# Optimization experiments

Measured on AMD Instinct MI355X. Metric: run time of the kernel, lower is better.

The kernel has to match this reference:

```python
import jax, jax.numpy as jnp
import numpy as np

B, T, D, H = 4, 1024, 1024, 16
DH = D // H
EPS = 1e-5


def setup_inputs() -> dict:
    key = jax.random.key(0)
    ks = jax.random.split(key, 14)
    sc = 1.0 / np.sqrt(D)
    x = jax.random.normal(ks[0], (B, T, D), jnp.float32)
    W_r = jax.random.normal(ks[1], (D, D), jnp.float32) * sc
    W_k = jax.random.normal(ks[2], (D, D), jnp.float32) * sc
    W_v = jax.random.normal(ks[3], (D, D), jnp.float32) * sc
    W_w = jax.random.normal(ks[4], (D, D), jnp.float32) * sc
    W_o = jax.random.normal(ks[5], (D, D), jnp.float32) * sc
    u = jax.random.normal(ks[6], (H, DH), jnp.float32) * 0.1
    tm_r = jax.random.uniform(ks[7], (D,), jnp.float32)
    tm_k = jax.random.uniform(ks[8], (D,), jnp.float32)
    tm_v = jax.random.uniform(ks[9], (D,), jnp.float32)
    tm_w = jax.random.uniform(ks[10], (D,), jnp.float32)
    ln_w = jnp.ones((DH,), jnp.float32) + 0.1 * jax.random.normal(ks[11], (DH,), jnp.float32)
    ln_b = 0.1 * jax.random.normal(ks[12], (DH,), jnp.float32)
    return {"x": x, "W_r": W_r, "W_k": W_k, "W_v": W_v, "W_w": W_w, "W_o": W_o,
            "u": u, "tm_r": tm_r, "tm_k": tm_k, "tm_v": tm_v, "tm_w": tm_w,
            "ln_w": ln_w, "ln_b": ln_b}


def _rwkv6(x, W_r, W_k, W_v, W_w, W_o, u, tm_r, tm_k, tm_v, tm_w, ln_w, ln_b):
    b, t, d = x.shape
    # token-shift mix
    x_prev = jnp.concatenate([jnp.zeros_like(x[:, :1]), x[:, :-1]], axis=1)
    xr = tm_r * x + (1.0 - tm_r) * x_prev
    xk = tm_k * x + (1.0 - tm_k) * x_prev
    xv = tm_v * x + (1.0 - tm_v) * x_prev
    xw = tm_w * x + (1.0 - tm_w) * x_prev
    r = jax.nn.sigmoid(xr @ W_r.T)          # (B,T,D)
    k = xk @ W_k.T
    v = xv @ W_v.T
    w = -jax.nn.softplus(-(xw @ W_w.T)) - 1e-4  # always < 0 -> exp(w) in (0,1)
    r = r.reshape(b, t, H, DH)
    k = k.reshape(b, t, H, DH)
    v = v.reshape(b, t, H, DH)
    w = w.reshape(b, t, H, DH)

    def step(s, rkvw):
        r_t, k_t, v_t, w_t = rkvw  # each (B,H,DH)
        bonus = jnp.exp(u + k_t)[..., :, None] * v_t[..., None, :]  # (B,H,DH,DH)
        o_t = jnp.einsum('bhi,bhij->bhj', r_t, s + bonus)
        s = jnp.exp(w_t)[..., None] * s + k_t[..., :, None] * v_t[..., None, :]
        return s, o_t

    s0 = jnp.zeros((b, H, DH, DH), x.dtype)
    rkvw = tuple(a.transpose(1, 0, 2, 3) for a in (r, k, v, w))  # (T,B,H,DH)
    _, o = jax.lax.scan(step, s0, rkvw)      # o: (T,B,H,DH)
    o = o.transpose(1, 0, 2, 3)              # (B,T,H,DH)
    # group LayerNorm over head dim
    mu = jnp.mean(o, axis=-1, keepdims=True)
    var = jnp.var(o, axis=-1, keepdims=True)
    o = (o - mu) * jax.lax.rsqrt(var + EPS) * ln_w + ln_b
    o = o * r
    return (o.reshape(b, t, d)) @ W_o.T


def reference(x, W_r, W_k, W_v, W_w, W_o, u, tm_r, tm_k, tm_v, tm_w, ln_w, ln_b):
    return _rwkv6(x, W_r, W_k, W_v, W_w, W_o, u, tm_r, tm_k, tm_v, tm_w, ln_w, ln_b)
```

## Files before the change

kernel.cpp:

```cpp
#include <hip/hip_runtime.h>


typedef unsigned short u16;
typedef unsigned int   u32;

typedef __attribute__((ext_vector_type(8))) __bf16 bf16x8;
typedef __attribute__((ext_vector_type(4))) float   f32x4;

#define MB (1u << 20)

#define LDS_PTR(p) ((__attribute__((address_space(3))) void*)(p))
#define GLB_PTR(p) ((const __attribute__((address_space(1))) void*)(p))

__device__ __forceinline__ u16 f2bf(float f) {
  u32 u = __builtin_bit_cast(u32, f);
  u += 0x7FFFu + ((u >> 16) & 1u);
  return (u16)(u >> 16);
}
__device__ __forceinline__ float bf2f(u16 x) {
  u32 u = ((u32)x) << 16;
  return __builtin_bit_cast(float, u);
}
__device__ __forceinline__ u32 pack2(float a, float b) {
  return (u32)f2bf(a) | ((u32)f2bf(b) << 16);
}

__global__ __launch_bounds__(256) void prep_w(
    const float* __restrict__ w0, const float* __restrict__ w1,
    const float* __restrict__ w2, const float* __restrict__ w3,
    const float* __restrict__ w4, u32* __restrict__ out) {
  int idx = blockIdx.x * 256 + threadIdx.x;
  int m = idx >> 19;
  int l = idx & 524287;
  const float* src = (m == 0) ? w0 : (m == 1) ? w1 : (m == 2) ? w2 : (m == 3) ? w3 : w4;
  float2 v = *(const float2*)(src + (size_t)l * 2);
  out[idx] = pack2(v.x, v.y);
}

__global__ __launch_bounds__(256) void prep_mix(
    const float* __restrict__ x,
    const float* __restrict__ tmr, const float* __restrict__ tmk,
    const float* __restrict__ tmv, const float* __restrict__ tmw,
    u32* __restrict__ xr, u32* __restrict__ xk,
    u32* __restrict__ xv, u32* __restrict__ xw) {
  int idx = blockIdx.x * 256 + threadIdx.x;
  int t  = (idx >> 9) & 1023;
  int d0 = (idx & 511) * 2;
  size_t e = (size_t)idx * 2;
  float2 xc = *(const float2*)(x + e);
  float2 xp = make_float2(0.f, 0.f);
  if (t > 0) xp = *(const float2*)(x + e - 1024);
  float2 tm;
  tm = *(const float2*)(tmr + d0);
  xr[idx] = pack2(tm.x * xc.x + (1.f - tm.x) * xp.x, tm.y * xc.y + (1.f - tm.y) * xp.y);
  tm = *(const float2*)(tmk + d0);
  xk[idx] = pack2(tm.x * xc.x + (1.f - tm.x) * xp.x, tm.y * xc.y + (1.f - tm.y) * xp.y);
  tm = *(const float2*)(tmv + d0);
  xv[idx] = pack2(tm.x * xc.x + (1.f - tm.x) * xp.x, tm.y * xc.y + (1.f - tm.y) * xp.y);
  tm = *(const float2*)(tmw + d0);
  xw[idx] = pack2(tm.x * xc.x + (1.f - tm.x) * xp.x, tm.y * xc.y + (1.f - tm.y) * xp.y);
}

__global__ __launch_bounds__(512, 1) void gemm_proj(
    const u16* __restrict__ xr, const u16* __restrict__ xk,
    const u16* __restrict__ xv, const u16* __restrict__ xw,
    const u16* __restrict__ Wr, const u16* __restrict__ Wk,
    const u16* __restrict__ Wv, const u16* __restrict__ Ww,
    u16* __restrict__ rO, u16* __restrict__ kO,
    u16* __restrict__ vO, float* __restrict__ wO) {
  constexpr int KITER = 16;
  constexpr int LDK   = 1024;
  __shared__ __align__(16) u16 Asm[2 * 16384];
  __shared__ __align__(16) u16 Bsm[2 * 16384];

  int mat = blockIdx.z;
  const u16* A = (mat == 0) ? xr : (mat == 1) ? xk : (mat == 2) ? xv : xw;
  const u16* W = (mat == 0) ? Wr : (mat == 1) ? Wk : (mat == 2) ? Wv : Ww;

  int tid = threadIdx.x;
  int m0 = blockIdx.x * 256, n0 = blockIdx.y * 256;
  int wave = tid >> 6, lane = tid & 63;
  int wm = (wave >> 2) * 128;
  int wn = (wave & 3) * 64;
  int r16 = lane & 15, quad = lane >> 4;

  f32x4 acc[8][4] = {};

  int lrow  = lane >> 3;
  int lchk  = (lane & 7) ^ lrow;
  const u16* Ag[4];
  const u16* Bg[4];
#pragma unroll
  for (int i = 0; i < 4; ++i) {
    int row = wave * 32 + i * 8 + lrow;
    Ag[i] = A + (size_t)(m0 + row) * LDK + lchk * 8;
    Bg[i] = W + (size_t)(n0 + row) * LDK + lchk * 8;
  }
  int ldsW = wave * 2048;

  int aoff[8], boff[4];
#pragma unroll
  for (int mt = 0; mt < 8; ++mt) {
    int r = wm + mt * 16 + r16;
    aoff[mt] = r * 64 + (quad ^ (r16 & 7)) * 8;
  }
#pragma unroll
  for (int nt = 0; nt < 4; ++nt) {
    int r = wn + nt * 16 + r16;
    boff[nt] = r * 64 + (quad ^ (r16 & 7)) * 8;
  }

#define ISSUE_TILE(t, buf)                                                              \
  do {                                                                                  \
    int _o = (buf) * 16384 + ldsW, _k = (t) * 64;                                       \
    __builtin_amdgcn_global_load_lds(GLB_PTR(Ag[0] + _k), LDS_PTR(Asm + _o),        16, 0, 0); \
    __builtin_amdgcn_global_load_lds(GLB_PTR(Ag[1] + _k), LDS_PTR(Asm + _o + 512),  16, 0, 0); \
    __builtin_amdgcn_global_load_lds(GLB_PTR(Ag[2] + _k), LDS_PTR(Asm + _o + 1024), 16, 0, 0); \
    __builtin_amdgcn_global_load_lds(GLB_PTR(Ag[3] + _k), LDS_PTR(Asm + _o + 1536), 16, 0, 0); \
    __builtin_amdgcn_global_load_lds(GLB_PTR(Bg[0] + _k), LDS_PTR(Bsm + _o),        16, 0, 0); \
    __builtin_amdgcn_global_load_lds(GLB_PTR(Bg[1] + _k), LDS_PTR(Bsm + _o + 512),  16, 0, 0); \
    __builtin_amdgcn_global_load_lds(GLB_PTR(Bg[2] + _k), LDS_PTR(Bsm + _o + 1024), 16, 0, 0); \
    __builtin_amdgcn_global_load_lds(GLB_PTR(Bg[3] + _k), LDS_PTR(Bsm + _o + 1536), 16, 0, 0); \
  } while (0)

  ISSUE_TILE(0, 0);
  ISSUE_TILE(1, 1);

  int cur = 0;
  for (int i = 0; i < KITER; ++i) {
    if (i < KITER - 1) asm volatile("s_waitcnt vmcnt(8)" ::: "memory");
    else               asm volatile("s_waitcnt vmcnt(0)" ::: "memory");
    __builtin_amdgcn_s_barrier();

    const u16* As = Asm + cur * 16384;
    const u16* Bs = Bsm + cur * 16384;
#pragma unroll
    for (int kk = 0; kk < 2; ++kk) {
      int kx = kk * 32;
      bf16x8 af[8], bfm[4];
#pragma unroll
      for (int mt = 0; mt < 8; ++mt) af[mt] = *(const bf16x8*)&As[aoff[mt] ^ kx];
#pragma unroll
      for (int nt = 0; nt < 4; ++nt) bfm[nt] = *(const bf16x8*)&Bs[boff[nt] ^ kx];
#pragma unroll
      for (int mt = 0; mt < 8; ++mt)
#pragma unroll
        for (int nt = 0; nt < 4; ++nt)
          acc[mt][nt] = __builtin_amdgcn_mfma_f32_16x16x32_bf16(af[mt], bfm[nt], acc[mt][nt], 0, 0, 0);
    }

    asm volatile("s_waitcnt lgkmcnt(0)" ::: "memory");
    __builtin_amdgcn_s_barrier();
    if (i + 2 < KITER) ISSUE_TILE(i + 2, cur);
    cur ^= 1;
  }
#undef ISSUE_TILE

#pragma unroll
  for (int mt = 0; mt < 8; ++mt) {
#pragma unroll
    for (int nt = 0; nt < 4; ++nt) {
#pragma unroll
      for (int rg = 0; rg < 4; ++rg) {
        int row = m0 + wm + mt * 16 + quad * 4 + rg;
        int col = n0 + wn + nt * 16 + r16;
        float v = acc[mt][nt][rg];
        size_t idx = (size_t)row * 1024 + col;
        if (mat == 0)      rO[idx] = f2bf(1.f / (1.f + __expf(-v)));
        else if (mat == 1) kO[idx] = f2bf(v);
        else if (mat == 2) vO[idx] = f2bf(v);
        else               wO[idx] = v;
      }
    }
  }
}

template <int KITER>
__device__ __forceinline__ void gemm_core(
    const u16* __restrict__ A, const u16* __restrict__ W, float* __restrict__ O,
    u16* Asm, u16* Bsm) {
  constexpr int LDK = KITER * 32;
  int tid = threadIdx.x;
  int m0 = blockIdx.x * 128, n0 = blockIdx.y * 128;
  int wave = tid >> 6, lane = tid & 63;
  int wm = (wave >> 1) * 64, wn = (wave & 1) * 64;
  int r16 = lane & 15, quad = lane >> 4;

  f32x4 acc[4][4] = {};

  int srow0 = wave * 32 + (lane >> 2);
  int srow1 = srow0 + 16;
  int c4    = lane & 3;
  int q0 = c4 ^ ((srow0 >> 1) & 3);
  int q1 = c4 ^ ((srow1 >> 1) & 3);
  const u16* Ag0 = A + (size_t)(m0 + srow0) * LDK + q0 * 8;
  const u16* Ag1 = A + (size_t)(m0 + srow1) * LDK + q1 * 8;
  const u16* Bg0 = W + (size_t)(n0 + srow0) * LDK + q0 * 8;
  const u16* Bg1 = W + (size_t)(n0 + srow1) * LDK + q1 * 8;
  int ldsOff0 = wave * 1024;
  int ldsOff1 = wave * 1024 + 512;

  int aoff[4], boff[4];
#pragma unroll
  for (int mt = 0; mt < 4; ++mt) {
    int r = wm + mt * 16 + r16;
    aoff[mt] = r * 32 + (quad ^ ((r >> 1) & 3)) * 8;
  }
#pragma unroll
  for (int nt = 0; nt < 4; ++nt) {
    int r = wn + nt * 16 + r16;
    boff[nt] = r * 32 + (quad ^ ((r >> 1) & 3)) * 8;
  }

#define ISSUE_TILE(t, buf)                                                              \
  do {                                                                                  \
    int _o = (buf) * 4096, _k = (t) * 32;                                               \
    __builtin_amdgcn_global_load_lds(GLB_PTR(Ag0 + _k), LDS_PTR(Asm + _o + ldsOff0), 16, 0, 0); \
    __builtin_amdgcn_global_load_lds(GLB_PTR(Ag1 + _k), LDS_PTR(Asm + _o + ldsOff1), 16, 0, 0); \
    __builtin_amdgcn_global_load_lds(GLB_PTR(Bg0 + _k), LDS_PTR(Bsm + _o + ldsOff0), 16, 0, 0); \
    __builtin_amdgcn_global_load_lds(GLB_PTR(Bg1 + _k), LDS_PTR(Bsm + _o + ldsOff1), 16, 0, 0); \
  } while (0)

  ISSUE_TILE(0, 0);
  ISSUE_TILE(1, 1);
  ISSUE_TILE(2, 2);

  int cur = 0;
  for (int i = 0; i < KITER; ++i) {
    if (i < KITER - 2)       asm volatile("s_waitcnt vmcnt(8)" ::: "memory");
    else if (i == KITER - 2) asm volatile("s_waitcnt vmcnt(4)" ::: "memory");
    else                     asm volatile("s_waitcnt vmcnt(0)" ::: "memory");
    __builtin_amdgcn_s_barrier();

    const u16* As = Asm + cur * 4096;
    const u16* Bs = Bsm + cur * 4096;
    bf16x8 af[4], bfm[4];
#pragma unroll
    for (int mt = 0; mt < 4; ++mt) af[mt] = *(const bf16x8*)&As[aoff[mt]];
#pragma unroll
    for (int nt = 0; nt < 4; ++nt) bfm[nt] = *(const bf16x8*)&Bs[boff[nt]];
#pragma unroll
    for (int mt = 0; mt < 4; ++mt)
#pragma unroll
      for (int nt = 0; nt < 4; ++nt)
        acc[mt][nt] = __builtin_amdgcn_mfma_f32_16x16x32_bf16(af[mt], bfm[nt], acc[mt][nt], 0, 0, 0);

    asm volatile("s_waitcnt lgkmcnt(0)" ::: "memory");
    __builtin_amdgcn_s_barrier();
    if (i + 3 < KITER) ISSUE_TILE(i + 3, cur);
    cur = (cur == 2) ? 0 : cur + 1;
  }
#undef ISSUE_TILE

#pragma unroll
  for (int mt = 0; mt < 4; ++mt)
#pragma unroll
    for (int nt = 0; nt < 4; ++nt)
#pragma unroll
      for (int rg = 0; rg < 4; ++rg) {
        int row = m0 + wm + mt * 16 + quad * 4 + rg;
        int col = n0 + wn + nt * 16 + r16;
        O[(size_t)row * 1024 + col] = acc[mt][nt][rg];
      }
}

__global__ __launch_bounds__(256) void gemm_out(
    const u16* __restrict__ A, const u16* __restrict__ W, float* __restrict__ O) {
  __shared__ __align__(16) u16 Asm[3 * 4096];
  __shared__ __align__(16) u16 Bsm[3 * 4096];
  gemm_core<32>(A, W, O, Asm, Bsm);
}

__global__ __launch_bounds__(256) void scan_intra(
    const u16* __restrict__ rb, const u16* __restrict__ kb,
    const u16* __restrict__ vb, const float* __restrict__ wb,
    const float* __restrict__ u,
    float* __restrict__ o, u16* __restrict__ rd,
    float* __restrict__ U, float* __restrict__ Dc) {
  int c = blockIdx.x, bh = blockIdx.y;
  int b = bh >> 4, h = bh & 15;
  int tid = threadIdx.x, ig = tid >> 6, j = tid & 63;

  __shared__ __align__(16) float4 combo[4][64];
  __shared__ float vs_[4][64];
  __shared__ float part[4][4][64];

  const float EW_SCALE = 0.99990001f;

  float s[16];
#pragma unroll
  for (int ii = 0; ii < 16; ++ii) s[ii] = 0.f;

  size_t base = ((size_t)(b * 1024 + c * 32)) * 1024 + h * 64 + j;
  float dloc = 1.0f;
  float uval = (ig < 2) ? u[h * 64 + j] : 0.f;

#define STAGE(t2, sl)                                                     \
  do {                                                                    \
    size_t _idx = base + (size_t)(t2) * 1024;                             \
    if (ig < 2) {                                                         \
      float _r = bf2f(rb[_idx]);                                          \
      float _k = bf2f(kb[_idx]);                                          \
      float _z = wb[_idx];                                                \
      combo[sl][j] = make_float4(_r, _k, __expf(uval + _k),               \
                                 EW_SCALE / (1.f + __expf(-_z)));         \
    } else {                                                              \
      vs_[sl][j] = bf2f(vb[_idx]);                                        \
    }                                                                     \
  } while (0)

  { int p = ig & 1; STAGE(p, p); }
  __syncthreads();

  for (int tt = 0; tt < 32; tt += 2) {
    if (tt + 2 < 32) {
      int p = ig & 1;
      int t2 = tt + 2 + p;
      STAGE(t2, t2 & 3);
    }
#pragma unroll
    for (int p = 0; p < 2; ++p) {
      int t = tt + p, sl = t & 3;
      float vj = vs_[sl][j];
      float acc = 0.f;
#pragma unroll
      for (int ii = 0; ii < 16; ++ii) {
        float4 cb = combo[sl][ig * 16 + ii];
        float tmp = fmaf(cb.z, vj, s[ii]);
        acc = fmaf(cb.x, tmp, acc);
        s[ii] = fmaf(cb.w, s[ii], cb.y * vj);
      }
      part[sl][ig][j] = acc;
      if (ig == 0) {
        float4 me = combo[sl][j];
        rd[base + (size_t)t * 1024] = f2bf(me.x * dloc);
        dloc *= me.w;
      }
    }
    if (tt >= 2) {
      if (ig == 2) {
        int t = tt - 2, sl = t & 3;
        o[base + (size_t)t * 1024] =
            part[sl][0][j] + part[sl][1][j] + part[sl][2][j] + part[sl][3][j];
      } else if (ig == 3) {
        int t = tt - 1, sl = t & 3;
        o[base + (size_t)t * 1024] =
            part[sl][0][j] + part[sl][1][j] + part[sl][2][j] + part[sl][3][j];
      }
    }
    __syncthreads();
  }
#undef STAGE
  if (ig == 2) {
    o[base + (size_t)30 * 1024] = part[2][0][j] + part[2][1][j] + part[2][2][j] + part[2][3][j];
  } else if (ig == 3) {
    o[base + (size_t)31 * 1024] = part[3][0][j] + part[3][1][j] + part[3][2][j] + part[3][3][j];
  }

  float* Ug = U + (size_t)(bh * 32 + c) * 4096;
#pragma unroll
  for (int ii = 0; ii < 16; ++ii) Ug[(ig * 16 + ii) * 64 + j] = s[ii];
  if (ig == 0) Dc[(bh * 32 + c) * 64 + j] = dloc;
}

__global__ __launch_bounds__(256) void state_prop(
    float* __restrict__ U, const float* __restrict__ Dc) {
  int bh  = blockIdx.x >> 4;
  int e   = (blockIdx.x & 15) * 256 + threadIdx.x;
  int i   = e >> 6;
  float acc = 0.f;
  for (int c = 0; c < 32; ++c) {
    float* Ug = U + (size_t)(bh * 32 + c) * 4096 + e;
    float d = Dc[(bh * 32 + c) * 64 + i];
    float uv = *Ug;
    *Ug = acc;
    acc = fmaf(d, acc, uv);
  }
}

__global__ __launch_bounds__(128) void inter_ln(
    const float* __restrict__ o, const u16* __restrict__ rd,
    const u16* __restrict__ rb, const float* __restrict__ U,
    const float* __restrict__ lnw, const float* __restrict__ lnb,
    u16* __restrict__ oh) {
  int c = blockIdx.x, bh = blockIdx.y;
  int b = bh >> 4, h = bh & 15;
  int tid = threadIdx.x, wave = tid >> 6, lane = tid & 63;
  int l15 = lane & 15, quad = lane >> 4;

  __shared__ __align__(16) u16 Sb[64][72];

  const float* Sg = U + (size_t)(bh * 32 + c) * 4096;
#pragma unroll
  for (int q = 0; q < 32; ++q) {
    int e = q * 128 + tid;
    Sb[e & 63][e >> 6] = f2bf(Sg[e]);
  }
  __syncthreads();

  size_t rbase = ((size_t)(b * 1024 + c * 32)) * 1024 + h * 64;

  const u16* rdg = rd + rbase + (size_t)(wave * 16 + l15) * 1024 + quad * 8;
  bf16x8 af0 = *(const bf16x8*)(rdg);
  bf16x8 af1 = *(const bf16x8*)(rdg + 32);

  f32x4 acc[4] = {};
#pragma unroll
  for (int nt = 0; nt < 4; ++nt) {
    const u16* bp = &Sb[nt * 16 + l15][quad * 8];
    bf16x8 b0 = *(const bf16x8*)bp;
    bf16x8 b1 = *(const bf16x8*)(bp + 32);
    acc[nt] = __builtin_amdgcn_mfma_f32_16x16x32_bf16(af0, b0, acc[nt], 0, 0, 0);
    acc[nt] = __builtin_amdgcn_mfma_f32_16x16x32_bf16(af1, b1, acc[nt], 0, 0, 0);
  }

#pragma unroll
  for (int rg = 0; rg < 4; ++rg) {
    int t = wave * 16 + quad * 4 + rg;
    size_t rowb = rbase + (size_t)t * 1024;
    float v[4];
    float s1 = 0.f, s2 = 0.f;
#pragma unroll
    for (int nt = 0; nt < 4; ++nt) {
      v[nt] = acc[nt][rg] + o[rowb + nt * 16 + l15];
      s1 += v[nt];
      s2 += v[nt] * v[nt];
    }
#pragma unroll
    for (int m = 1; m < 16; m <<= 1) {
      s1 += __shfl_xor(s1, m, 64);
      s2 += __shfl_xor(s2, m, 64);
    }
    float mu  = s1 * (1.f / 64.f);
    float var = s2 * (1.f / 64.f) - mu * mu;
    float rstd = rsqrtf(var + 1e-5f);
#pragma unroll
    for (int nt = 0; nt < 4; ++nt) {
      int jj = nt * 16 + l15;
      float nv = (v[nt] - mu) * rstd;
      float val = (nv * lnw[jj] + lnb[jj]) * bf2f(rb[rowb + jj]);
      oh[rowb + jj] = f2bf(val);
    }
  }
}

extern "C" void kernel_launch(void* const* d_in, const int* in_sizes, int n_in,
                              void* d_out, int out_size, void* d_ws, size_t ws_size,
                              hipStream_t stream) {
  const float* x    = (const float*)d_in[0];
  const float* W_r  = (const float*)d_in[1];
  const float* W_k  = (const float*)d_in[2];
  const float* W_v  = (const float*)d_in[3];
  const float* W_w  = (const float*)d_in[4];
  const float* W_o  = (const float*)d_in[5];
  const float* u    = (const float*)d_in[6];
  const float* tm_r = (const float*)d_in[7];
  const float* tm_k = (const float*)d_in[8];
  const float* tm_v = (const float*)d_in[9];
  const float* tm_w = (const float*)d_in[10];
  const float* ln_w = (const float*)d_in[11];
  const float* ln_b = (const float*)d_in[12];
  float* out = (float*)d_out;

  char* ws = (char*)d_ws;
  u16* xr = (u16*)(ws + (size_t)0 * MB);
  u16* xk = (u16*)(ws + (size_t)8 * MB);
  u16* xv = (u16*)(ws + (size_t)16 * MB);
  u16* xw = (u16*)(ws + (size_t)24 * MB);
  float* Ubuf = (float*)(ws + (size_t)0 * MB);
  u16* Wb = (u16*)(ws + (size_t)32 * MB);
  u16* Wrb = Wb;
  u16* Wkb = (u16*)(ws + (size_t)34 * MB);
  u16* Wvb = (u16*)(ws + (size_t)36 * MB);
  u16* Wwb = (u16*)(ws + (size_t)38 * MB);
  u16* Wob = (u16*)(ws + (size_t)40 * MB);
  float* Dcbuf = (float*)(ws + (size_t)42 * MB);
  u16*   rbuf = (u16*)(ws + (size_t)48 * MB);
  u16*   kbuf = (u16*)(ws + (size_t)56 * MB);
  u16*   vbuf = (u16*)(ws + (size_t)64 * MB);
  float* wbuf = (float*)(ws + (size_t)72 * MB);
  float* obuf = (float*)(ws + (size_t)88 * MB);
  u16*  rdbuf = (u16*)(ws + (size_t)104 * MB);
  u16*   ohbuf = (u16*)(ws + (size_t)129 * MB);

  prep_w<<<10240, 256, 0, stream>>>(W_r, W_k, W_v, W_w, W_o, (u32*)Wb);
  prep_mix<<<8192, 256, 0, stream>>>(x, tm_r, tm_k, tm_v, tm_w,
                                     (u32*)xr, (u32*)xk, (u32*)xv, (u32*)xw);
  gemm_proj<<<dim3(16, 4, 4), 512, 0, stream>>>(xr, xk, xv, xw,
                                                Wrb, Wkb, Wvb, Wwb,
                                                rbuf, kbuf, vbuf, wbuf);
  scan_intra<<<dim3(32, 64), 256, 0, stream>>>(rbuf, kbuf, vbuf, wbuf, u,
                                               obuf, rdbuf, Ubuf, Dcbuf);
  state_prop<<<1024, 256, 0, stream>>>(Ubuf, Dcbuf);
  inter_ln<<<dim3(32, 64), 128, 0, stream>>>(obuf, rdbuf, rbuf, Ubuf,
                                             ln_w, ln_b, ohbuf);
  gemm_out<<<dim3(32, 8, 1), 256, 0, stream>>>(ohbuf, Wob, out);
}
```

Baseline: 257.3 us.

## Retile intra-chunk scan state as 4x4 register blocks per thread

```diff
diff --git a/kernel.cpp b/kernel.cpp
--- a/kernel.cpp
+++ b/kernel.cpp
@@ -279,88 +279,119 @@
     float* __restrict__ U, float* __restrict__ Dc) {
   int c = blockIdx.x, bh = blockIdx.y;
   int b = bh >> 4, h = bh & 15;
-  int tid = threadIdx.x, ig = tid >> 6, j = tid & 63;
+  int tid = threadIdx.x;
+  int wave = tid >> 6, lane = tid & 63;
+  int ig4 = tid >> 4, jq = tid & 15;
 
   __shared__ __align__(16) float4 combo[4][64];
-  __shared__ float vs_[4][64];
-  __shared__ float part[4][4][64];
+  __shared__ __align__(16) float4 vs4[4][16];
+  __shared__ __align__(16) float  part[4][16][68];
 
   const float EW_SCALE = 0.99990001f;
 
-  float s[16];
-#pragma unroll
-  for (int ii = 0; ii < 16; ++ii) s[ii] = 0.f;
-
-  size_t base = ((size_t)(b * 1024 + c * 32)) * 1024 + h * 64 + j;
+  float s[4][4];
+#pragma unroll
+  for (int ii = 0; ii < 4; ++ii)
+#pragma unroll
+    for (int jj = 0; jj < 4; ++jj) s[ii][jj] = 0.f;
+
+  size_t base = ((size_t)(b * 1024 + c * 32)) * 1024 + h * 64 + lane;
   float dloc = 1.0f;
-  float uval = (ig < 2) ? u[h * 64 + j] : 0.f;
+  float uval = (wave < 2) ? u[h * 64 + lane] : 0.f;
 
 #define STAGE(t2, sl)                                                     \
   do {                                                                    \
     size_t _idx = base + (size_t)(t2) * 1024;                             \
-    if (ig < 2) {                                                         \
+    if (wave < 2) {                                                       \
       float _r = bf2f(rb[_idx]);                                          \
       float _k = bf2f(kb[_idx]);                                          \
       float _z = wb[_idx];                                                \
-      combo[sl][j] = make_float4(_r, _k, __expf(uval + _k),               \
-                                 EW_SCALE / (1.f + __expf(-_z)));         \
+      combo[sl][lane] = make_float4(_r, _k, __expf(uval + _k),            \
+                                    EW_SCALE / (1.f + __expf(-_z)));      \
     } else {                                                              \
-      vs_[sl][j] = bf2f(vb[_idx]);                                        \
+      ((float*)vs4)[(sl) * 64 + lane] = bf2f(vb[_idx]);                   \
     }                                                                     \
   } while (0)
 
-  { int p = ig & 1; STAGE(p, p); }
+  { int p = wave & 1; STAGE(p, p); }
   __syncthreads();
 
   for (int tt = 0; tt < 32; tt += 2) {
     if (tt + 2 < 32) {
-      int p = ig & 1;
+      int p = wave & 1;
       int t2 = tt + 2 + p;
       STAGE(t2, t2 & 3);
     }
 #pragma unroll
     for (int p = 0; p < 2; ++p) {
       int t = tt + p, sl = t & 3;
-      float vj = vs_[sl][j];
-      float acc = 0.f;
-#pragma unroll
-      for (int ii = 0; ii < 16; ++ii) {
-        float4 cb = combo[sl][ig * 16 + ii];
-        float tmp = fmaf(cb.z, vj, s[ii]);
-        acc = fmaf(cb.x, tmp, acc);
-        s[ii] = fmaf(cb.w, s[ii], cb.y * vj);
-      }
-      part[sl][ig][j] = acc;
-      if (ig == 0) {
-        float4 me = combo[sl][j];
+      float4 vv = vs4[sl][jq];
+      float4 cb0 = combo[sl][ig4 * 4 + 0];
+      float4 cb1 = combo[sl][ig4 * 4 + 1];
+      float4 cb2 = combo[sl][ig4 * 4 + 2];
+      float4 cb3 = combo[sl][ig4 * 4 + 3];
+      float ac0 = 0.f, ac1 = 0.f, ac2 = 0.f, ac3 = 0.f;
+#define ROW(cb, ii)                                                       \
+      do {                                                                \
+        float t0 = fmaf(cb.z, vv.x, s[ii][0]);                            \
+        float t1 = fmaf(cb.z, vv.y, s[ii][1]);                            \
+        float t2_ = fmaf(cb.z, vv.z, s[ii][2]);                           \
+        float t3 = fmaf(cb.z, vv.w, s[ii][3]);                            \
+        ac0 = fmaf(cb.x, t0, ac0);                                        \
+        ac1 = fmaf(cb.x, t1, ac1);                                        \
+        ac2 = fmaf(cb.x, t2_, ac2);                                       \
+        ac3 = fmaf(cb.x, t3, ac3);                                        \
+        s[ii][0] = fmaf(cb.w, s[ii][0], cb.y * vv.x);                     \
+        s[ii][1] = fmaf(cb.w, s[ii][1], cb.y * vv.y);                     \
+        s[ii][2] = fmaf(cb.w, s[ii][2], cb.y * vv.z);                     \
+        s[ii][3] = fmaf(cb.w, s[ii][3], cb.y * vv.w);                     \
+      } while (0)
+      ROW(cb0, 0); ROW(cb1, 1); ROW(cb2, 2); ROW(cb3, 3);
+#undef ROW
+      *(float4*)&part[sl][ig4][jq * 4] = make_float4(ac0, ac1, ac2, ac3);
+      if (wave == 0) {
+        float4 me = combo[sl][lane];
         rd[base + (size_t)t * 1024] = f2bf(me.x * dloc);
         dloc *= me.w;
       }
     }
     if (tt >= 2) {
-      if (ig == 2) {
+      if (wave == 2) {
         int t = tt - 2, sl = t & 3;
-        o[base + (size_t)t * 1024] =
-            part[sl][0][j] + part[sl][1][j] + part[sl][2][j] + part[sl][3][j];
-      } else if (ig == 3) {
+        float sum = 0.f;
+#pragma unroll
+        for (int g = 0; g < 16; ++g) sum += part[sl][g][lane];
+        o[base + (size_t)t * 1024] = sum;
+      } else if (wave == 3) {
         int t = tt - 1, sl = t & 3;
-        o[base + (size_t)t * 1024] =
-            part[sl][0][j] + part[sl][1][j] + part[sl][2][j] + part[sl][3][j];
+        float sum = 0.f;
+#pragma unroll
+        for (int g = 0; g < 16; ++g) sum += part[sl][g][lane];
+        o[base + (size_t)t * 1024] = sum;
       }
     }
     __syncthreads();
   }
 #undef STAGE
-  if (ig == 2) {
-    o[base + (size_t)30 * 1024] = part[2][0][j] + part[2][1][j] + part[2][2][j] + part[2][3][j];
-  } else if (ig == 3) {
-    o[base + (size_t)31 * 1024] = part[3][0][j] + part[3][1][j] + part[3][2][j] + part[3][3][j];
+  if (wave == 2) {
+    float sum = 0.f;
+#pragma unroll
+    for (int g = 0; g < 16; ++g) sum += part[2][g][lane];
+    o[base + (size_t)30 * 1024] = sum;
+  } else if (wave == 3) {
+    float sum = 0.f;
+#pragma unroll
+    for (int g = 0; g < 16; ++g) sum += part[3][g][lane];
+    o[base + (size_t)31 * 1024] = sum;
   }
 
   float* Ug = U + (size_t)(bh * 32 + c) * 4096;
 #pragma unroll
-  for (int ii = 0; ii < 16; ++ii) Ug[(ig * 16 + ii) * 64 + j] = s[ii];
-  if (ig == 0) Dc[(bh * 32 + c) * 64 + j] = dloc;
+  for (int ii = 0; ii < 4; ++ii) {
+    *(float4*)&Ug[(ig4 * 4 + ii) * 64 + jq * 4] =
+        make_float4(s[ii][0], s[ii][1], s[ii][2], s[ii][3]);
+  }
+  if (wave == 0) Dc[(bh * 32 + c) * 64 + lane] = dloc;
 }
 
 __global__ __launch_bounds__(256) void state_prop(
```

Result: faster. 242.8 us (-5.6%).
